# Performance work log

Measured on AMD Instinct MI355X. Metric: run time of the kernel, lower is better.

The kernel has to match this reference:

```python
import jax, jax.numpy as jnp
import numpy as np

PAD = 1
ORDERS = ['back', 'down', 'front', 'left', 'right', 'top']
# connected face for each of ['up','down','left','right'] sides (from self.relation)
NEIGHBORS = {
    'back':  ['top', 'down', 'right', 'left'],
    'down':  ['front', 'back', 'left', 'right'],
    'front': ['top', 'down', 'left', 'right'],
    'left':  ['top', 'down', 'back', 'front'],
    'right': ['top', 'down', 'front', 'back'],
    'top':   ['back', 'front', 'left', 'right'],
}
SIDES = ['up', 'down', 'left', 'right']

def _rot_y(t):
    c, s = np.cos(t), np.sin(t)
    return np.array([[c, 0, s], [0, 1, 0], [-s, 0, c]], np.float64)

def _rot_x(t):
    c, s = np.cos(t), np.sin(t)
    return np.array([[1, 0, 0], [0, c, -s], [0, s, c]], np.float64)

def _precompute(h, pad):
    # Reconstruction of Equirec2Cube geometry used by SpherePad._GetLoc.
    # Padded cube face has side Wp = h + 2*pad and FOV theta = 2*arctan((0.5h+pad)/(0.5h)).
    Wp = h + 2 * pad
    cxp = (Wp - 1) / 2.0
    tan_half = (0.5 * h + pad) / (0.5 * h)  # tan(theta/2)
    fp = cxp / tan_half                      # focal of padded cube (pixel-edge convention)
    u = (np.arange(Wp) - cxp) / fp
    gx, gy = np.meshgrid(u, u)              # x right, y down, camera looks along +z
    grid = np.stack([gx, gy, np.ones_like(gx)], axis=-1)  # [Wp, Wp, 3] front-face rays
    # world->camera rotations per face, ordered/named to match ORDERS
    R = {'back': _rot_y(np.pi), 'down': _rot_x(np.pi / 2), 'front': np.eye(3),
         'left': _rot_y(np.pi / 2), 'right': _rot_y(-np.pi / 2), 'top': _rot_x(-np.pi / 2)}
    data = {}
    for face in ORDERS:
        data[face] = {}
        for j, side in enumerate(SIDES):
            conn = NEIGHBORS[face][j]
            Rrel = R[conn] @ R[face].T       # self-cam -> connected-cam
            g = grid @ Rrel.T                # [Wp, Wp, 3]
            # original FOV=90 K has f == cx, so normalized grid_sample coord = X/Z, Y/Z
            x = g[..., 0] / g[..., 2]
            y = g[..., 1] / g[..., 2]
            mask = (x >= -1.01) & (x <= 1.01) & (y >= -1.01) & (y <= 1.01)
            xy = np.clip(np.stack([x, y], axis=-1), -1.0, 1.0).astype(np.float32)
            if side == 'up':
                sl = (slice(0, pad), slice(None))
            elif side == 'down':
                sl = (slice(Wp - pad, Wp), slice(None))
            elif side == 'left':
                sl = (slice(None), slice(0, pad))
            else:
                sl = (slice(None), slice(Wp - pad, Wp))
            data[face][side] = (xy[sl], mask[sl])
    return data

def _grid_sample(img, grid):
    # img [N,C,H,W], grid [N,Hg,Wg,2] in [-1,1]; bilinear, align_corners=True
    N, C, H, W = img.shape
    x = (grid[..., 0] + 1.0) * 0.5 * (W - 1)
    y = (grid[..., 1] + 1.0) * 0.5 * (H - 1)
    x0 = jnp.floor(x)
    y0 = jnp.floor(y)
    wx = (x - x0)[..., None]
    wy = (y - y0)[..., None]
    x0i = jnp.clip(x0.astype(jnp.int32), 0, W - 1)
    x1i = jnp.clip(x0i + 1, 0, W - 1)
    y0i = jnp.clip(y0.astype(jnp.int32), 0, H - 1)
    y1i = jnp.clip(y0i + 1, 0, H - 1)
    b = jnp.arange(N)[:, None, None]
    v00 = img[b, :, y0i, x0i]  # [N,Hg,Wg,C]
    v01 = img[b, :, y0i, x1i]
    v10 = img[b, :, y1i, x0i]
    v11 = img[b, :, y1i, x1i]
    out = (v00 * (1 - wx) * (1 - wy) + v01 * wx * (1 - wy)
           + v10 * (1 - wx) * wy + v11 * wx * wy)
    return out.transpose(0, 3, 1, 2)  # [N,C,Hg,Wg]

def _forward(inputs, pad):
    bs, c, h, w = inputs.shape
    rep = bs // 6
    data = _precompute(h, pad)       # numpy constants, computed at trace time
    faces = inputs.reshape(rep, 6, c, h, w)   # inputs[i::6] == faces[:, i]
    outs = []
    for i, face in enumerate(ORDERS):
        tf = jnp.pad(faces[:, i], ((0, 0), (0, 0), (pad, pad), (pad, pad)))
        for j, side in enumerate(SIDES):
            conn = faces[:, ORDERS.index(NEIGHBORS[face][j])]
            xy, mask = data[face][side]
            grid = jnp.broadcast_to(jnp.asarray(xy), (rep,) + xy.shape)
            interp = _grid_sample(conn, grid)          # [rep,c,strip_h,strip_w]
            m = jnp.asarray(mask)[None, None]
            if side == 'up':
                tf = tf.at[:, :, :pad, :].set(jnp.where(m, interp, tf[:, :, :pad, :]))
            elif side == 'down':
                tf = tf.at[:, :, -pad:, :].set(jnp.where(m, interp, tf[:, :, -pad:, :]))
            elif side == 'left':
                tf = tf.at[:, :, :, :pad].set(jnp.where(m, interp, tf[:, :, :, :pad]))
            else:
                tf = tf.at[:, :, :, -pad:].set(jnp.where(m, interp, tf[:, :, :, -pad:]))
        outs.append(tf)
    # torch: cat by face then re-interleave -> out[k*6+i] = face i of panorama k
    return jnp.stack(outs, axis=1).reshape(bs, c, h + 2 * pad, w + 2 * pad)

def setup_inputs() -> dict:
    key = jax.random.key(0)
    inputs = jax.random.normal(key, (24, 256, 128, 128), dtype=jnp.float32)
    return {'inputs': inputs}

def reference(inputs):
    return _forward(inputs, PAD)
```

## Files before the change

### kernel.cpp

```cpp
#include <hip/hip_runtime.h>

#define H    128
#define WP   130
#define NCH  256
#define NB   24

__constant__ int c_R[6][9] = {
  {-1,0,0,  0,1,0,  0,0,-1},
  { 1,0,0,  0,0,-1, 0,1,0 },
  { 1,0,0,  0,1,0,  0,0,1 },
  { 0,0,1,  0,1,0, -1,0,0 },
  { 0,0,-1, 0,1,0,  1,0,0 },
  { 1,0,0,  0,0,1,  0,-1,0},
};

__constant__ int c_conn[6][4] = {
  {5,1,4,3},
  {2,0,3,4},
  {5,1,3,4},
  {5,1,0,2},
  {5,1,2,0},
  {0,2,3,4},
};

#define INV_FP (65.0f / 4128.0f)

__global__ void __launch_bounds__(256)
interior_kernel(const float4* __restrict__ in4, float* __restrict__ out) {
  unsigned t = blockIdx.x * 256u + threadIdx.x;
  unsigned c4  = t & 31u;
  unsigned r   = (t >> 5) & 127u;
  unsigned img = t >> 12;
  float4 v = in4[t];
  unsigned o = img * 16900u + (r + 1u) * 130u + 1u + (c4 << 2);
  out[o]     = v.x;
  out[o + 1] = v.y;
  out[o + 2] = v.z;
  out[o + 3] = v.w;
}

__global__ void __launch_bounds__(256)
border_kernel(const float* __restrict__ in, float* __restrict__ out) {
  unsigned tid = blockIdx.x * 256u + threadIdx.x;
  const unsigned total = 6144u * 516u;
  if (tid >= total) return;

  unsigned img = tid / 516u;
  unsigned k   = tid - img * 516u;

  int r, c;
  if (k < 130u)      { r = 0;              c = (int)k; }
  else if (k < 260u) { r = WP - 1;         c = (int)(k - 130u); }
  else if (k < 388u) { r = (int)(k - 259u); c = 0; }
  else               { r = (int)(k - 387u); c = WP - 1; }

  int n    = (int)(img >> 8);
  int ch   = (int)(img & 255u);
  int face = n % 6;
  int rep  = n / 6;
  float v  = 0.0f;

  int cand[2]; int nc = 0;
  if (c == WP - 1) cand[nc++] = 3;
  if (c == 0)      cand[nc++] = 2;
  if (r == WP - 1) cand[nc++] = 1;
  if (r == 0)      cand[nc++] = 0;

  float uc = ((float)c - 64.5f) * INV_FP;
  float ur = ((float)r - 64.5f) * INV_FP;

  for (int kk = 0; kk < nc; ++kk) {
    int s  = cand[kk];
    int cf = c_conn[face][s];
    const int* Rc = c_R[cf];
    const int* Rf = c_R[face];
    float g[3];
    #pragma unroll
    for (int i = 0; i < 3; ++i) {
      float acc = 0.0f;
      #pragma unroll
      for (int j = 0; j < 3; ++j) {
        int rr = Rc[i*3+0]*Rf[j*3+0] + Rc[i*3+1]*Rf[j*3+1] + Rc[i*3+2]*Rf[j*3+2];
        float dj = (j == 0) ? uc : (j == 1) ? ur : 1.0f;
        acc += (float)rr * dj;
      }
      g[i] = acc;
    }
    float x = g[0] / g[2];
    float y = g[1] / g[2];
    if (fabsf(x) <= 1.01f && fabsf(y) <= 1.01f) {
      x = fminf(fmaxf(x, -1.0f), 1.0f);
      y = fminf(fmaxf(y, -1.0f), 1.0f);
      const float* src = in + ((size_t)((rep * 6 + cf) * NCH + ch)) * H * H;
      float xp = (x + 1.0f) * 0.5f * (float)(H - 1);
      float yp = (y + 1.0f) * 0.5f * (float)(H - 1);
      float x0 = floorf(xp), y0 = floorf(yp);
      float wx = xp - x0,    wy = yp - y0;
      int x0i = min(max((int)x0, 0), H - 1);
      int x1i = min(x0i + 1, H - 1);
      int y0i = min(max((int)y0, 0), H - 1);
      int y1i = min(y0i + 1, H - 1);
      float v00 = src[y0i * H + x0i];
      float v01 = src[y0i * H + x1i];
      float v10 = src[y1i * H + x0i];
      float v11 = src[y1i * H + x1i];
      v = v00 * (1.0f - wx) * (1.0f - wy)
        + v01 * wx          * (1.0f - wy)
        + v10 * (1.0f - wx) * wy
        + v11 * wx          * wy;
      break;
    }
  }
  out[(unsigned)img * 16900u + (unsigned)r * 130u + (unsigned)c] = v;
}

extern "C" void kernel_launch(void* const* d_in, const int* in_sizes, int n_in,
                              void* d_out, int out_size, void* d_ws, size_t ws_size,
                              hipStream_t stream) {
  (void)in_sizes; (void)n_in; (void)d_ws; (void)ws_size; (void)out_size;
  const float* in = (const float*)d_in[0];
  float* out = (float*)d_out;

  interior_kernel<<<98304, 256, 0, stream>>>((const float4*)in, out);

  const unsigned btotal  = 6144u * 516u;
  const unsigned bblocks = (btotal + 255u) / 256u;
  border_kernel<<<bblocks, 256, 0, stream>>>(in, out);
}
```

Before: 270.9 us.

## Fuse interior copy and border sampling into one output-major kernel with table

Replaces the separate interior-copy and border-sampling kernels with a single kernel in which each thread writes four consecutive output floats as one float4, so stores are aligned and vectorised instead of scattered scalar writes at an odd row stride. Border pixels use a small per-face table, built by a tiny kernel in the workspace, that holds the source face, four bilinear indices and weights, so the per-pixel rotation math is no longer done for every channel. The interior reads become unaligned scalar loads, the table is rebuilt on every call, and the old path is kept as a fallback when the workspace is too small.

```diff
diff --git a/kernel.cpp b/kernel.cpp
--- a/kernel.cpp
+++ b/kernel.cpp
@@ -4,6 +4,10 @@
 #define WP   130
 #define NCH  256
 #define NB   24
+#define NIMG 6144
+#define QPI  4225
+#define BPF  516
+#define TBLN 3096
 
 __constant__ int c_R[6][9] = {
   {-1,0,0,  0,1,0,  0,0,-1},
@@ -13,52 +17,29 @@
   { 0,0,-1, 0,1,0,  1,0,0 },
   { 1,0,0,  0,0,1,  0,-1,0},
 };
-
 __constant__ int c_conn[6][4] = {
-  {5,1,4,3},
-  {2,0,3,4},
-  {5,1,3,4},
-  {5,1,0,2},
-  {5,1,2,0},
-  {0,2,3,4},
+  {5,1,4,3}, {2,0,3,4}, {5,1,3,4}, {5,1,0,2}, {5,1,2,0}, {0,2,3,4},
 };
 
 #define INV_FP (65.0f / 4128.0f)
 
 __global__ void __launch_bounds__(256)
-interior_kernel(const float4* __restrict__ in4, float* __restrict__ out) {
-  unsigned t = blockIdx.x * 256u + threadIdx.x;
-  unsigned c4  = t & 31u;
-  unsigned r   = (t >> 5) & 127u;
-  unsigned img = t >> 12;
-  float4 v = in4[t];
-  unsigned o = img * 16900u + (r + 1u) * 130u + 1u + (c4 << 2);
-  out[o]     = v.x;
-  out[o + 1] = v.y;
-  out[o + 2] = v.z;
-  out[o + 3] = v.w;
-}
-
-__global__ void __launch_bounds__(256)
-border_kernel(const float* __restrict__ in, float* __restrict__ out) {
-  unsigned tid = blockIdx.x * 256u + threadIdx.x;
-  const unsigned total = 6144u * 516u;
-  if (tid >= total) return;
-
-  unsigned img = tid / 516u;
-  unsigned k   = tid - img * 516u;
+border_table_kernel(int* __restrict__ tb_face, int4* __restrict__ tb_idx,
+                    float4* __restrict__ tb_w) {
+  int t = blockIdx.x * 256 + threadIdx.x;
+  if (t >= TBLN) return;
+  int face = t / BPF;
+  int k    = t - face * BPF;
 
   int r, c;
-  if (k < 130u)      { r = 0;              c = (int)k; }
-  else if (k < 260u) { r = WP - 1;         c = (int)(k - 130u); }
-  else if (k < 388u) { r = (int)(k - 259u); c = 0; }
-  else               { r = (int)(k - 387u); c = WP - 1; }
-
-  int n    = (int)(img >> 8);
-  int ch   = (int)(img & 255u);
-  int face = n % 6;
-  int rep  = n / 6;
-  float v  = 0.0f;
+  if (k < 130)      { r = 0;        c = k; }
+  else if (k < 260) { r = WP - 1;   c = k - 130; }
+  else if (k < 388) { r = k - 259;  c = 0; }
+  else              { r = k - 387;  c = WP - 1; }
+
+  int fs = -1;
+  int4  idx = make_int4(0, 0, 0, 0);
+  float4 w  = make_float4(0.f, 0.f, 0.f, 0.f);
 
   int cand[2]; int nc = 0;
   if (c == WP - 1) cand[nc++] = 3;
@@ -91,7 +72,6 @@
     if (fabsf(x) <= 1.01f && fabsf(y) <= 1.01f) {
       x = fminf(fmaxf(x, -1.0f), 1.0f);
       y = fminf(fmaxf(y, -1.0f), 1.0f);
-      const float* src = in + ((size_t)((rep * 6 + cf) * NCH + ch)) * H * H;
       float xp = (x + 1.0f) * 0.5f * (float)(H - 1);
       float yp = (y + 1.0f) * 0.5f * (float)(H - 1);
       float x0 = floorf(xp), y0 = floorf(yp);
@@ -100,14 +80,128 @@
       int x1i = min(x0i + 1, H - 1);
       int y0i = min(max((int)y0, 0), H - 1);
       int y1i = min(y0i + 1, H - 1);
-      float v00 = src[y0i * H + x0i];
-      float v01 = src[y0i * H + x1i];
-      float v10 = src[y1i * H + x0i];
-      float v11 = src[y1i * H + x1i];
-      v = v00 * (1.0f - wx) * (1.0f - wy)
-        + v01 * wx          * (1.0f - wy)
-        + v10 * (1.0f - wx) * wy
-        + v11 * wx          * wy;
+      fs  = cf;
+      idx = make_int4(y0i * H + x0i, y0i * H + x1i, y1i * H + x0i, y1i * H + x1i);
+      w   = make_float4((1.f - wx) * (1.f - wy), wx * (1.f - wy),
+                        (1.f - wx) * wy,         wx * wy);
+      break;
+    }
+  }
+  tb_face[t] = fs;
+  tb_idx[t]  = idx;
+  tb_w[t]    = w;
+}
+
+__global__ void __launch_bounds__(256)
+spherepad_out_kernel(const float* __restrict__ in, float4* __restrict__ out4,
+                     const int* __restrict__ tb_face,
+                     const int4* __restrict__ tb_idx,
+                     const float4* __restrict__ tb_w) {
+  unsigned q   = blockIdx.x * 256u + threadIdx.x;
+  unsigned img = blockIdx.y;
+  if (q >= QPI) return;
+
+  unsigned p       = q << 2;
+  unsigned base_in = img << 14;
+  unsigned n       = img >> 8;
+  unsigned ch      = img & 255u;
+  unsigned rep     = n / 6u;
+  unsigned face    = n - rep * 6u;
+
+  float vals[4];
+  #pragma unroll
+  for (int j = 0; j < 4; ++j) {
+    unsigned pj = p + (unsigned)j;
+    unsigned r  = pj / 130u;
+    unsigned c  = pj - r * 130u;
+    if ((r - 1u) < 128u && (c - 1u) < 128u) {
+      vals[j] = in[base_in + ((r - 1u) << 7) + (c - 1u)];
+    } else {
+      unsigned tk = (r == 0u)   ? c
+                  : (r == 129u) ? (130u + c)
+                  : (c == 0u)   ? (259u + r)
+                  :               (387u + r);
+      unsigned ti = face * (unsigned)BPF + tk;
+      int fs = tb_face[ti];
+      float v = 0.0f;
+      if (fs >= 0) {
+        int4   id = tb_idx[ti];
+        float4 w  = tb_w[ti];
+        unsigned src = (((rep * 6u + (unsigned)fs) << 8) + ch) << 14;
+        v = w.x * in[src + (unsigned)id.x]
+          + w.y * in[src + (unsigned)id.y]
+          + w.z * in[src + (unsigned)id.z]
+          + w.w * in[src + (unsigned)id.w];
+      }
+      vals[j] = v;
+    }
+  }
+  out4[img * (unsigned)QPI + q] = make_float4(vals[0], vals[1], vals[2], vals[3]);
+}
+
+__global__ void __launch_bounds__(256)
+interior_kernel(const float4* __restrict__ in4, float* __restrict__ out) {
+  unsigned t = blockIdx.x * 256u + threadIdx.x;
+  unsigned c4  = t & 31u;
+  unsigned r   = (t >> 5) & 127u;
+  unsigned img = t >> 12;
+  float4 v = in4[t];
+  unsigned o = img * 16900u + (r + 1u) * 130u + 1u + (c4 << 2);
+  out[o] = v.x; out[o + 1] = v.y; out[o + 2] = v.z; out[o + 3] = v.w;
+}
+
+__global__ void __launch_bounds__(256)
+border_kernel(const float* __restrict__ in, float* __restrict__ out) {
+  unsigned tid = blockIdx.x * 256u + threadIdx.x;
+  const unsigned total = 6144u * 516u;
+  if (tid >= total) return;
+  unsigned img = tid / 516u;
+  unsigned k   = tid - img * 516u;
+  int r, c;
+  if (k < 130u)      { r = 0;               c = (int)k; }
+  else if (k < 260u) { r = WP - 1;          c = (int)(k - 130u); }
+  else if (k < 388u) { r = (int)(k - 259u); c = 0; }
+  else               { r = (int)(k - 387u); c = WP - 1; }
+  int n = (int)(img >> 8), ch = (int)(img & 255u);
+  int face = n % 6, rep = n / 6;
+  float v = 0.0f;
+  int cand[2]; int nc = 0;
+  if (c == WP - 1) cand[nc++] = 3;
+  if (c == 0)      cand[nc++] = 2;
+  if (r == WP - 1) cand[nc++] = 1;
+  if (r == 0)      cand[nc++] = 0;
+  float uc = ((float)c - 64.5f) * INV_FP;
+  float ur = ((float)r - 64.5f) * INV_FP;
+  for (int kk = 0; kk < nc; ++kk) {
+    int s = cand[kk], cf = c_conn[face][s];
+    const int* Rc = c_R[cf]; const int* Rf = c_R[face];
+    float g[3];
+    #pragma unroll
+    for (int i = 0; i < 3; ++i) {
+      float acc = 0.0f;
+      #pragma unroll
+      for (int j = 0; j < 3; ++j) {
+        int rr = Rc[i*3+0]*Rf[j*3+0] + Rc[i*3+1]*Rf[j*3+1] + Rc[i*3+2]*Rf[j*3+2];
+        float dj = (j == 0) ? uc : (j == 1) ? ur : 1.0f;
+        acc += (float)rr * dj;
+      }
+      g[i] = acc;
+    }
+    float x = g[0] / g[2], y = g[1] / g[2];
+    if (fabsf(x) <= 1.01f && fabsf(y) <= 1.01f) {
+      x = fminf(fmaxf(x, -1.0f), 1.0f);
+      y = fminf(fmaxf(y, -1.0f), 1.0f);
+      const float* src = in + ((size_t)((rep * 6 + cf) * NCH + ch)) * H * H;
+      float xp = (x + 1.0f) * 0.5f * (float)(H - 1);
+      float yp = (y + 1.0f) * 0.5f * (float)(H - 1);
+      float x0 = floorf(xp), y0 = floorf(yp);
+      float wx = xp - x0, wy = yp - y0;
+      int x0i = min(max((int)x0, 0), H - 1);
+      int x1i = min(x0i + 1, H - 1);
+      int y0i = min(max((int)y0, 0), H - 1);
+      int y1i = min(y0i + 1, H - 1);
+      v = src[y0i*H+x0i]*(1.f-wx)*(1.f-wy) + src[y0i*H+x1i]*wx*(1.f-wy)
+        + src[y1i*H+x0i]*(1.f-wx)*wy       + src[y1i*H+x1i]*wx*wy;
       break;
     }
   }
@@ -117,13 +211,22 @@
 extern "C" void kernel_launch(void* const* d_in, const int* in_sizes, int n_in,
                               void* d_out, int out_size, void* d_ws, size_t ws_size,
                               hipStream_t stream) {
-  (void)in_sizes; (void)n_in; (void)d_ws; (void)ws_size; (void)out_size;
+  (void)in_sizes; (void)n_in; (void)out_size;
   const float* in = (const float*)d_in[0];
   float* out = (float*)d_out;
 
-  interior_kernel<<<98304, 256, 0, stream>>>((const float4*)in, out);
-
-  const unsigned btotal  = 6144u * 516u;
-  const unsigned bblocks = (btotal + 255u) / 256u;
-  border_kernel<<<bblocks, 256, 0, stream>>>(in, out);
-}
+  const size_t need = (size_t)TBLN * (4 + 16 + 16);
+  if (d_ws != nullptr && ws_size >= need) {
+    int*    tb_face = (int*)d_ws;
+    int4*   tb_idx  = (int4*)(tb_face + TBLN);
+    float4* tb_w    = (float4*)(tb_idx + TBLN);
+    border_table_kernel<<<(TBLN + 255) / 256, 256, 0, stream>>>(tb_face, tb_idx, tb_w);
+    dim3 grid((QPI + 255) / 256, NIMG);
+    spherepad_out_kernel<<<grid, 256, 0, stream>>>(in, (float4*)out,
+                                                   tb_face, tb_idx, tb_w);
+  } else {
+    interior_kernel<<<98304, 256, 0, stream>>>((const float4*)in, out);
+    const unsigned btotal = 6144u * 516u;
+    border_kernel<<<(btotal + 255u) / 256u, 256, 0, stream>>>(in, out);
+  }
+}
```

New measurement: 414.1 us. 52.8% more time.
